# Performance work log

Measured on AMD Instinct MI355X. Metric: run time of the kernel, lower is better.

## Reference

```python
import jax, jax.numpy as jnp
import numpy as np

N_NODES = 50000
N_EDGES = 600000
D_IN = 128
D_HID = 1024
D_OUT = 128


def setup_inputs() -> dict:
    key = jax.random.key(0)
    ks = jax.random.split(key, 8)
    feat = jax.random.normal(ks[0], (N_NODES, D_IN), dtype=jnp.float32)
    edge_feat = jax.random.normal(ks[1], (N_EDGES, D_IN), dtype=jnp.float32)
    src = jax.random.randint(ks[2], (N_EDGES,), 0, N_NODES, dtype=jnp.int32)
    dst = jax.random.randint(ks[3], (N_EDGES,), 0, N_NODES, dtype=jnp.int32)
    W1 = jax.random.normal(ks[4], (D_IN, D_HID), dtype=jnp.float32) * (1.0 / np.sqrt(D_IN))
    b1 = jnp.zeros((D_HID,), dtype=jnp.float32)
    W2 = jax.random.normal(ks[5], (D_HID, D_OUT), dtype=jnp.float32) * (1.0 / np.sqrt(D_HID))
    b2 = jnp.zeros((D_OUT,), dtype=jnp.float32)
    return {"feat": feat, "edge_feat": edge_feat, "src": src, "dst": dst,
            "W1": W1, "b1": b1, "W2": W2, "b2": b2}


def reference(feat, edge_feat, src, dst, W1, b1, W2, b2):
    # DGL u_add_e: message m_e = h_src(e) + e_feat(e)   [E, D_IN]
    messages = feat[src] + edge_feat
    # reduce sum over incoming edges at each destination node -> [N, D_IN]
    h = jax.ops.segment_sum(messages, dst, num_segments=N_NODES)
    # 2-layer MLP
    h = jax.nn.relu(h @ W1 + b1)
    return h @ W2 + b2
```

## Files before the change

kernel.cpp:

```cpp
#include <hip/hip_runtime.h>
#include <hip/hip_bf16.h>

#define N_NODES 50000
#define N_EDGES 600000
#define D_IN    128
#define D_HID   1024
#define D_OUT   128

#define WS_EID    12800000
#define WS_OFF    15200000
#define WS_CURSOR 15400016
#define WS_DEG    15600016
#define WS_BSUM   15800016
#define WS_W1T    15801040
#define WS_W2T    16063184

typedef short bf16x8 __attribute__((ext_vector_type(8)));
typedef float f32x4  __attribute__((ext_vector_type(4)));

__global__ __launch_bounds__(256) void hist_kernel(
    const int* __restrict__ dst, int* __restrict__ deg)
{
    int e = blockIdx.x * blockDim.x + threadIdx.x;
    if (e < N_EDGES) atomicAdd(&deg[dst[e]], 1);
}

__global__ __launch_bounds__(256) void scan1_kernel(
    const int* __restrict__ deg, int* __restrict__ bsum)
{
    __shared__ int red[256];
    int t = threadIdx.x;
    int idx = blockIdx.x * 256 + t;
    red[t] = (idx < N_NODES) ? deg[idx] : 0;
    __syncthreads();
    for (int s = 128; s > 0; s >>= 1) {
        if (t < s) red[t] += red[t + s];
        __syncthreads();
    }
    if (t == 0) bsum[blockIdx.x] = red[0];
}

#define SCAN_NB 196
__global__ __launch_bounds__(256) void scan2_kernel(
    int* __restrict__ bsum, int* __restrict__ off)
{
    __shared__ int sh[256];
    int t = threadIdx.x;
    int v = (t < SCAN_NB) ? bsum[t] : 0;
    sh[t] = v;
    __syncthreads();
    for (int ofs = 1; ofs < 256; ofs <<= 1) {
        int u = (t >= ofs) ? sh[t - ofs] : 0;
        __syncthreads();
        sh[t] += u;
        __syncthreads();
    }
    if (t < SCAN_NB) bsum[t] = sh[t] - v;
    if (t == 255) off[N_NODES] = sh[255];
}

__global__ __launch_bounds__(256) void scan3_kernel(
    const int* __restrict__ deg, const int* __restrict__ bsum,
    int* __restrict__ off, int* __restrict__ cursor)
{
    __shared__ int sh[256];
    int t = threadIdx.x;
    int idx = blockIdx.x * 256 + t;
    int v = (idx < N_NODES) ? deg[idx] : 0;
    sh[t] = v;
    __syncthreads();
    for (int ofs = 1; ofs < 256; ofs <<= 1) {
        int u = (t >= ofs) ? sh[t - ofs] : 0;
        __syncthreads();
        sh[t] += u;
        __syncthreads();
    }
    if (idx < N_NODES) {
        int ex = bsum[blockIdx.x] + sh[t] - v;
        off[idx] = ex;
        cursor[idx] = ex;
    }
}

__global__ __launch_bounds__(256) void fill_kernel(
    const int* __restrict__ dst, int* __restrict__ cursor, int* __restrict__ eid)
{
    int e = blockIdx.x * blockDim.x + threadIdx.x;
    if (e < N_EDGES) {
        int pos = atomicAdd(&cursor[dst[e]], 1);
        eid[pos] = e;
    }
}

__global__ __launch_bounds__(256) void transpose_cvt2_kernel(
    const float* __restrict__ W1, __hip_bfloat16* __restrict__ w1t,
    const float* __restrict__ W2, __hip_bfloat16* __restrict__ w2t)
{
    __shared__ float tile[32][33];
    int b = blockIdx.x;
    const float* in;
    __hip_bfloat16* outp;
    int rows, cols, c0, r0;
    if (b < 128) {
        in = W1; outp = w1t; rows = D_IN; cols = D_HID;
        c0 = (b & 31) * 32; r0 = (b >> 5) * 32;
    } else {
        int bb = b - 128;
        in = W2; outp = w2t; rows = D_HID; cols = D_OUT;
        c0 = (bb & 3) * 32; r0 = (bb >> 2) * 32;
    }
    int tx = threadIdx.x & 31, ty = threadIdx.x >> 5;
    #pragma unroll
    for (int i = 0; i < 32; i += 8)
        tile[ty + i][tx] = in[(size_t)(r0 + ty + i) * cols + (c0 + tx)];
    __syncthreads();
    #pragma unroll
    for (int i = 0; i < 32; i += 8)
        outp[(size_t)(c0 + ty + i) * rows + (r0 + tx)] =
            __float2bfloat16(tile[tx][ty + i]);
}

#define HS_STRIDE 136
#define QS_STRIDE 72

__global__ __launch_bounds__(256) void fused_gnn_kernel(
    const float* __restrict__ feat,
    const float* __restrict__ edge_feat,
    const int*   __restrict__ src,
    const int*   __restrict__ eid,
    const int*   __restrict__ off,
    const __hip_bfloat16* __restrict__ w1t,
    const float* __restrict__ b1,
    const __hip_bfloat16* __restrict__ w2t,
    const float* __restrict__ b2,
    float* __restrict__ out)
{
    __shared__ __align__(16) short h_s[64 * HS_STRIDE];
    __shared__ __align__(16) short q_s[2][64 * QS_STRIDE];

    const int t    = threadIdx.x;
    const int wv   = t >> 6;
    const int lane = t & 63;
    const int half = lane >> 4;
    const int lid  = lane & 15;
    const int nb   = blockIdx.x * 64;

    const short* w1s = (const short*)w1t;
    const short* w2s = (const short*)w2t;

    for (int j = 0; j < 16; ++j) {
        const int r = wv * 16 + j;
        const int n = nb + r;
        float2 a0 = make_float2(0.f, 0.f), a1 = a0, a2 = a0, a3 = a0;
        if (n < N_NODES) {
            int i   = __builtin_amdgcn_readfirstlane(off[n]);
            int end = __builtin_amdgcn_readfirstlane(off[n + 1]);
            for (; i + 3 < end; i += 4) {
                int e0 = __builtin_amdgcn_readfirstlane(eid[i]);
                int e1 = __builtin_amdgcn_readfirstlane(eid[i + 1]);
                int e2 = __builtin_amdgcn_readfirstlane(eid[i + 2]);
                int e3 = __builtin_amdgcn_readfirstlane(eid[i + 3]);
                int s0 = __builtin_amdgcn_readfirstlane(src[e0]);
                int s1 = __builtin_amdgcn_readfirstlane(src[e1]);
                int s2 = __builtin_amdgcn_readfirstlane(src[e2]);
                int s3 = __builtin_amdgcn_readfirstlane(src[e3]);
                float2 f0 = ((const float2*)(edge_feat + (size_t)e0 * D_IN))[lane];
                float2 g0 = ((const float2*)(feat      + (size_t)s0 * D_IN))[lane];
                float2 f1 = ((const float2*)(edge_feat + (size_t)e1 * D_IN))[lane];
                float2 g1 = ((const float2*)(feat      + (size_t)s1 * D_IN))[lane];
                float2 f2 = ((const float2*)(edge_feat + (size_t)e2 * D_IN))[lane];
                float2 g2 = ((const float2*)(feat      + (size_t)s2 * D_IN))[lane];
                float2 f3 = ((const float2*)(edge_feat + (size_t)e3 * D_IN))[lane];
                float2 g3 = ((const float2*)(feat      + (size_t)s3 * D_IN))[lane];
                a0.x += f0.x + g0.x;  a0.y += f0.y + g0.y;
                a1.x += f1.x + g1.x;  a1.y += f1.y + g1.y;
                a2.x += f2.x + g2.x;  a2.y += f2.y + g2.y;
                a3.x += f3.x + g3.x;  a3.y += f3.y + g3.y;
            }
            for (; i < end; ++i) {
                int e = __builtin_amdgcn_readfirstlane(eid[i]);
                int s = __builtin_amdgcn_readfirstlane(src[e]);
                float2 f = ((const float2*)(edge_feat + (size_t)e * D_IN))[lane];
                float2 g = ((const float2*)(feat      + (size_t)s * D_IN))[lane];
                a0.x += f.x + g.x;  a0.y += f.y + g.y;
            }
        }
        float sx = (a0.x + a1.x) + (a2.x + a3.x);
        float sy = (a0.y + a1.y) + (a2.y + a3.y);
        __hip_bfloat162 hv;
        hv.x = __float2bfloat16(sx);
        hv.y = __float2bfloat16(sy);
        *(__hip_bfloat162*)&h_s[r * HS_STRIDE + lane * 2] = hv;
    }
    __syncthreads();

    bf16x8 afrag[4][4];
    #pragma unroll
    for (int mt = 0; mt < 4; ++mt)
        #pragma unroll
        for (int ks = 0; ks < 4; ++ks)
            afrag[mt][ks] = *(const bf16x8*)&h_s[(mt * 16 + lid) * HS_STRIDE + ks * 32 + half * 8];

    f32x4 acc[4][2];
    #pragma unroll
    for (int mt = 0; mt < 4; ++mt) {
        acc[mt][0] = f32x4{0.f, 0.f, 0.f, 0.f};
        acc[mt][1] = f32x4{0.f, 0.f, 0.f, 0.f};
    }

    const int ncol1 = wv * 16 + lid;

    int pb = 0;
    for (int jb = 0; jb < D_HID; jb += 64, pb ^= 1) {
        float bias = b1[jb + ncol1];
        bf16x8 bfrag[4];
        #pragma unroll
        for (int ks = 0; ks < 4; ++ks)
            bfrag[ks] = *(const bf16x8*)&w1s[(size_t)(jb + ncol1) * 128 + ks * 32 + half * 8];

        f32x4 c1[4];
        #pragma unroll
        for (int mt = 0; mt < 4; ++mt) {
            f32x4 c = f32x4{bias, bias, bias, bias};
            #pragma unroll
            for (int ks = 0; ks < 4; ++ks)
                c = __builtin_amdgcn_mfma_f32_16x16x32_bf16(afrag[mt][ks], bfrag[ks], c, 0, 0, 0);
            c1[mt] = c;
        }

        #pragma unroll
        for (int mt = 0; mt < 4; ++mt) {
            #pragma unroll
            for (int r = 0; r < 4; ++r) {
                float v = fmaxf(c1[mt][r], 0.f);
                __hip_bfloat16 bv = __float2bfloat16(v);
                q_s[pb][(mt * 16 + half * 4 + r) * QS_STRIDE + wv * 16 + lid] = *(short*)&bv;
            }
        }
        __syncthreads();

        bf16x8 a2f[4][2];
        #pragma unroll
        for (int mt = 0; mt < 4; ++mt)
            #pragma unroll
            for (int ks = 0; ks < 2; ++ks)
                a2f[mt][ks] = *(const bf16x8*)&q_s[pb][(mt * 16 + lid) * QS_STRIDE + ks * 32 + half * 8];

        #pragma unroll
        for (int nt = 0; nt < 2; ++nt) {
            #pragma unroll
            for (int ks = 0; ks < 2; ++ks) {
                bf16x8 b2f = *(const bf16x8*)&w2s[(size_t)(wv * 32 + nt * 16 + lid) * 1024 + jb + ks * 32 + half * 8];
                #pragma unroll
                for (int mt = 0; mt < 4; ++mt)
                    acc[mt][nt] = __builtin_amdgcn_mfma_f32_16x16x32_bf16(a2f[mt][ks], b2f, acc[mt][nt], 0, 0, 0);
            }
        }
    }

    #pragma unroll
    for (int nt = 0; nt < 2; ++nt) {
        int col = wv * 32 + nt * 16 + lid;
        float bv = b2[col];
        #pragma unroll
        for (int mt = 0; mt < 4; ++mt) {
            #pragma unroll
            for (int r = 0; r < 4; ++r) {
                int row = nb + mt * 16 + half * 4 + r;
                if (row < N_NODES)
                    out[(size_t)row * D_OUT + col] = acc[mt][nt][r] + bv;
            }
        }
    }
}

extern "C" void kernel_launch(void* const* d_in, const int* in_sizes, int n_in,
                              void* d_out, int out_size, void* d_ws, size_t ws_size,
                              hipStream_t stream) {
    const float* feat      = (const float*)d_in[0];
    const float* edge_feat = (const float*)d_in[1];
    const int*   src       = (const int*)d_in[2];
    const int*   dst       = (const int*)d_in[3];
    const float* W1        = (const float*)d_in[4];
    const float* b1        = (const float*)d_in[5];
    const float* W2        = (const float*)d_in[6];
    const float* b2        = (const float*)d_in[7];
    float* out = (float*)d_out;

    char* ws = (char*)d_ws;
    int*   eid    = (int*)(ws + WS_EID);
    int*   off    = (int*)(ws + WS_OFF);
    int*   cursor = (int*)(ws + WS_CURSOR);
    int*   deg    = (int*)(ws + WS_DEG);
    int*   bsum   = (int*)(ws + WS_BSUM);
    __hip_bfloat16* w1t = (__hip_bfloat16*)(ws + WS_W1T);
    __hip_bfloat16* w2t = (__hip_bfloat16*)(ws + WS_W2T);

    hipMemsetAsync(deg, 0, (size_t)N_NODES * sizeof(int), stream);

    hist_kernel<<<(N_EDGES + 255) / 256, 256, 0, stream>>>(dst, deg);
    scan1_kernel<<<SCAN_NB, 256, 0, stream>>>(deg, bsum);
    scan2_kernel<<<1, 256, 0, stream>>>(bsum, off);
    scan3_kernel<<<SCAN_NB, 256, 0, stream>>>(deg, bsum, off, cursor);
    fill_kernel<<<(N_EDGES + 255) / 256, 256, 0, stream>>>(dst, cursor, eid);

    transpose_cvt2_kernel<<<256, 256, 0, stream>>>(W1, w1t, W2, w2t);

    fused_gnn_kernel<<<(N_NODES + 63) / 64, 256, 0, stream>>>(
        feat, edge_feat, src, eid, off, w1t, b1, w2t, b2, out);
}
```

Measured before the change: 655.5 us.

## Store (edge, src) pairs in CSR and gather two edges per wave with float4

The fill kernel now writes packed (edge id, src) pairs into the CSR array. The gather loop therefore no longer chases eid and then src through two dependent scalar loads. Each wave processes two edges at once, using each 32-lane half with float4 loads, and combines the halves with a cross-half shuffle. Node offsets are preloaded once per wave and broadcast with shuffles. The aim is shorter dependent-load chains and wider memory transactions, at the cost of more vector registers, a larger pair array, and extra shuffle reductions.

```diff
diff --git a/kernel.cpp b/kernel.cpp
--- a/kernel.cpp
+++ b/kernel.cpp
@@ -7,16 +7,18 @@
 #define D_HID   1024
 #define D_OUT   128
 
-#define WS_EID    12800000
-#define WS_OFF    15200000
-#define WS_CURSOR 15400016
-#define WS_DEG    15600016
-#define WS_BSUM   15800016
-#define WS_W1T    15801040
-#define WS_W2T    16063184
+#define WS_PAIRS  0
+#define WS_OFF    4800000
+#define WS_CURSOR 5000016
+#define WS_DEG    5200016
+#define WS_BSUM   5400016
+#define WS_W1T    5401040
+#define WS_W2T    5663184
 
 typedef short bf16x8 __attribute__((ext_vector_type(8)));
+typedef short s16x4  __attribute__((ext_vector_type(4)));
 typedef float f32x4  __attribute__((ext_vector_type(4)));
+typedef int   i32x2  __attribute__((ext_vector_type(2)));
 
 __global__ __launch_bounds__(256) void hist_kernel(
     const int* __restrict__ dst, int* __restrict__ deg)
@@ -83,12 +85,15 @@
 }
 
 __global__ __launch_bounds__(256) void fill_kernel(
-    const int* __restrict__ dst, int* __restrict__ cursor, int* __restrict__ eid)
+    const int* __restrict__ dst, const int* __restrict__ src,
+    int* __restrict__ cursor, int* __restrict__ pairs)
 {
     int e = blockIdx.x * blockDim.x + threadIdx.x;
     if (e < N_EDGES) {
+        int s = src[e];
         int pos = atomicAdd(&cursor[dst[e]], 1);
-        eid[pos] = e;
+        i32x2 v; v.x = e; v.y = s;
+        *(i32x2*)(pairs + 2 * (size_t)pos) = v;
     }
 }
 
@@ -126,8 +131,7 @@
 __global__ __launch_bounds__(256) void fused_gnn_kernel(
     const float* __restrict__ feat,
     const float* __restrict__ edge_feat,
-    const int*   __restrict__ src,
-    const int*   __restrict__ eid,
+    const int*   __restrict__ pairs,
     const int*   __restrict__ off,
     const __hip_bfloat16* __restrict__ w1t,
     const float* __restrict__ b1,
@@ -148,49 +152,74 @@
     const short* w1s = (const short*)w1t;
     const short* w2s = (const short*)w2t;
 
+    const int eh = lane >> 5;
+    const int ln = lane & 31;
+
+    int my_off = 0;
+    {
+        int oidx = nb + wv * 16 + lane;
+        if (lane <= 16) {
+            int c = oidx > N_NODES ? N_NODES : oidx;
+            my_off = off[c];
+        }
+    }
+
     for (int j = 0; j < 16; ++j) {
         const int r = wv * 16 + j;
-        const int n = nb + r;
-        float2 a0 = make_float2(0.f, 0.f), a1 = a0, a2 = a0, a3 = a0;
-        if (n < N_NODES) {
-            int i   = __builtin_amdgcn_readfirstlane(off[n]);
-            int end = __builtin_amdgcn_readfirstlane(off[n + 1]);
-            for (; i + 3 < end; i += 4) {
-                int e0 = __builtin_amdgcn_readfirstlane(eid[i]);
-                int e1 = __builtin_amdgcn_readfirstlane(eid[i + 1]);
-                int e2 = __builtin_amdgcn_readfirstlane(eid[i + 2]);
-                int e3 = __builtin_amdgcn_readfirstlane(eid[i + 3]);
-                int s0 = __builtin_amdgcn_readfirstlane(src[e0]);
-                int s1 = __builtin_amdgcn_readfirstlane(src[e1]);
-                int s2 = __builtin_amdgcn_readfirstlane(src[e2]);
-                int s3 = __builtin_amdgcn_readfirstlane(src[e3]);
-                float2 f0 = ((const float2*)(edge_feat + (size_t)e0 * D_IN))[lane];
-                float2 g0 = ((const float2*)(feat      + (size_t)s0 * D_IN))[lane];
-                float2 f1 = ((const float2*)(edge_feat + (size_t)e1 * D_IN))[lane];
-                float2 g1 = ((const float2*)(feat      + (size_t)s1 * D_IN))[lane];
-                float2 f2 = ((const float2*)(edge_feat + (size_t)e2 * D_IN))[lane];
-                float2 g2 = ((const float2*)(feat      + (size_t)s2 * D_IN))[lane];
-                float2 f3 = ((const float2*)(edge_feat + (size_t)e3 * D_IN))[lane];
-                float2 g3 = ((const float2*)(feat      + (size_t)s3 * D_IN))[lane];
-                a0.x += f0.x + g0.x;  a0.y += f0.y + g0.y;
-                a1.x += f1.x + g1.x;  a1.y += f1.y + g1.y;
-                a2.x += f2.x + g2.x;  a2.y += f2.y + g2.y;
-                a3.x += f3.x + g3.x;  a3.y += f3.y + g3.y;
+        int base = __builtin_amdgcn_readfirstlane(__shfl(my_off, j));
+        int end  = __builtin_amdgcn_readfirstlane(__shfl(my_off, j + 1));
+
+        f32x4 a0 = f32x4{0.f,0.f,0.f,0.f}, a1 = a0, a2 = a0, a3 = a0;
+        int i = base;
+        for (; i + 8 <= end; i += 8) {
+            i32x2 p0 = *(const i32x2*)(pairs + 2 * (size_t)(i + 0 + eh));
+            i32x2 p1 = *(const i32x2*)(pairs + 2 * (size_t)(i + 2 + eh));
+            i32x2 p2 = *(const i32x2*)(pairs + 2 * (size_t)(i + 4 + eh));
+            i32x2 p3 = *(const i32x2*)(pairs + 2 * (size_t)(i + 6 + eh));
+            f32x4 e0 = *(const f32x4*)(edge_feat + (size_t)p0.x * D_IN + ln * 4);
+            f32x4 g0 = *(const f32x4*)(feat      + (size_t)p0.y * D_IN + ln * 4);
+            f32x4 e1 = *(const f32x4*)(edge_feat + (size_t)p1.x * D_IN + ln * 4);
+            f32x4 g1 = *(const f32x4*)(feat      + (size_t)p1.y * D_IN + ln * 4);
+            f32x4 e2 = *(const f32x4*)(edge_feat + (size_t)p2.x * D_IN + ln * 4);
+            f32x4 g2 = *(const f32x4*)(feat      + (size_t)p2.y * D_IN + ln * 4);
+            f32x4 e3 = *(const f32x4*)(edge_feat + (size_t)p3.x * D_IN + ln * 4);
+            f32x4 g3 = *(const f32x4*)(feat      + (size_t)p3.y * D_IN + ln * 4);
+            a0 += e0 + g0;
+            a1 += e1 + g1;
+            a2 += e2 + g2;
+            a3 += e3 + g3;
+        }
+        for (; i + 4 <= end; i += 4) {
+            i32x2 p0 = *(const i32x2*)(pairs + 2 * (size_t)(i + 0 + eh));
+            i32x2 p1 = *(const i32x2*)(pairs + 2 * (size_t)(i + 2 + eh));
+            f32x4 e0 = *(const f32x4*)(edge_feat + (size_t)p0.x * D_IN + ln * 4);
+            f32x4 g0 = *(const f32x4*)(feat      + (size_t)p0.y * D_IN + ln * 4);
+            f32x4 e1 = *(const f32x4*)(edge_feat + (size_t)p1.x * D_IN + ln * 4);
+            f32x4 g1 = *(const f32x4*)(feat      + (size_t)p1.y * D_IN + ln * 4);
+            a0 += e0 + g0;
+            a1 += e1 + g1;
+        }
+        for (; i < end; i += 2) {
+            if (i + eh < end) {
+                i32x2 p = *(const i32x2*)(pairs + 2 * (size_t)(i + eh));
+                f32x4 e = *(const f32x4*)(edge_feat + (size_t)p.x * D_IN + ln * 4);
+                f32x4 g = *(const f32x4*)(feat      + (size_t)p.y * D_IN + ln * 4);
+                a0 += e + g;
             }
-            for (; i < end; ++i) {
-                int e = __builtin_amdgcn_readfirstlane(eid[i]);
-                int s = __builtin_amdgcn_readfirstlane(src[e]);
-                float2 f = ((const float2*)(edge_feat + (size_t)e * D_IN))[lane];
-                float2 g = ((const float2*)(feat      + (size_t)s * D_IN))[lane];
-                a0.x += f.x + g.x;  a0.y += f.y + g.y;
-            }
-        }
-        float sx = (a0.x + a1.x) + (a2.x + a3.x);
-        float sy = (a0.y + a1.y) + (a2.y + a3.y);
-        __hip_bfloat162 hv;
-        hv.x = __float2bfloat16(sx);
-        hv.y = __float2bfloat16(sy);
-        *(__hip_bfloat162*)&h_s[r * HS_STRIDE + lane * 2] = hv;
+        }
+        f32x4 s = (a0 + a1) + (a2 + a3);
+        s[0] += __shfl_xor(s[0], 32);
+        s[1] += __shfl_xor(s[1], 32);
+        s[2] += __shfl_xor(s[2], 32);
+        s[3] += __shfl_xor(s[3], 32);
+        if (eh == 0) {
+            s16x4 hv;
+            __hip_bfloat16 b0 = __float2bfloat16(s[0]); hv[0] = *(short*)&b0;
+            __hip_bfloat16 c1 = __float2bfloat16(s[1]); hv[1] = *(short*)&c1;
+            __hip_bfloat16 c2 = __float2bfloat16(s[2]); hv[2] = *(short*)&c2;
+            __hip_bfloat16 c3 = __float2bfloat16(s[3]); hv[3] = *(short*)&c3;
+            *(s16x4*)&h_s[r * HS_STRIDE + ln * 4] = hv;
+        }
     }
     __syncthreads();
 
@@ -288,7 +317,7 @@
     float* out = (float*)d_out;
 
     char* ws = (char*)d_ws;
-    int*   eid    = (int*)(ws + WS_EID);
+    int*   pairs  = (int*)(ws + WS_PAIRS);
     int*   off    = (int*)(ws + WS_OFF);
     int*   cursor = (int*)(ws + WS_CURSOR);
     int*   deg    = (int*)(ws + WS_DEG);
@@ -302,10 +331,10 @@
     scan1_kernel<<<SCAN_NB, 256, 0, stream>>>(deg, bsum);
     scan2_kernel<<<1, 256, 0, stream>>>(bsum, off);
     scan3_kernel<<<SCAN_NB, 256, 0, stream>>>(deg, bsum, off, cursor);
-    fill_kernel<<<(N_EDGES + 255) / 256, 256, 0, stream>>>(dst, cursor, eid);
+    fill_kernel<<<(N_EDGES + 255) / 256, 256, 0, stream>>>(dst, src, cursor, pairs);
 
     transpose_cvt2_kernel<<<256, 256, 0, stream>>>(W1, w1t, W2, w2t);
 
     fused_gnn_kernel<<<(N_NODES + 63) / 64, 256, 0, stream>>>(
-        feat, edge_feat, src, eid, off, w1t, b1, w2t, b2, out);
-}
+        feat, edge_feat, pairs, off, w1t, b1, w2t, b2, out);
+}
```

Result: faster. 636.1 us (-3.0%).
